# Kernel optimization log

Hardware: AMD Instinct MI355X
Metric: run time of the kernel (lower is better)

## Reference

```python
import jax, jax.numpy as jnp
import numpy as np

D_IN = 1024
D_OUT = 1024
N = 4096


def setup_inputs() -> dict:
    key = jax.random.key(0)
    kx, kq, kk, kv = jax.random.split(key, 4)
    x = jax.random.normal(kx, (N, D_IN), dtype=jnp.float32)
    # weights stored as [d_in, d_out] so that x @ W == torch Linear(x)
    s = 1.0 / np.sqrt(D_IN)
    W_q = jax.random.uniform(kq, (D_IN, D_OUT), jnp.float32, -s, s)
    W_k = jax.random.uniform(kk, (D_IN, D_OUT), jnp.float32, -s, s)
    W_v = jax.random.uniform(kv, (D_IN, D_OUT), jnp.float32, -s, s)
    return {"x": x, "W_q": W_q, "W_k": W_k, "W_v": W_v}


def reference(x, W_q, W_k, W_v):
    # x: [N, d_in]; projections -> [N, d_out]
    q = x @ W_q
    k = x @ W_k
    v = x @ W_v
    scale = 1.0 / jnp.sqrt(jnp.asarray(k.shape[-1], dtype=q.dtype))
    scores = (q @ k.T) * scale            # [N, N]
    weights = jax.nn.softmax(scores, axis=-1)
    return weights @ v                     # [N, d_out]
```

## Files before the change

kernel.cpp:

```cpp
#include <hip/hip_runtime.h>
#include <math.h>

typedef _Float16 f16;
typedef __attribute__((ext_vector_type(8))) _Float16 f16x8;
typedef __attribute__((ext_vector_type(4))) _Float16 f16x4;
typedef __attribute__((ext_vector_type(4))) float f32x4;

#define NSEQ 4096
#define DIN 1024
#define DOUT 1024

__device__ __forceinline__ void load16(const void* g, void* l) {
    __builtin_amdgcn_global_load_lds(
        (const __attribute__((address_space(1))) unsigned int*)g,
        (__attribute__((address_space(3))) unsigned int*)l, 16, 0, 0);
}

#define SB() __builtin_amdgcn_sched_barrier(0)
#define BARRIER() __builtin_amdgcn_s_barrier()

#define MM(I, J, KH, AR) \
    acc[I][J] = __builtin_amdgcn_mfma_f32_16x16x32_f16(AR[KH], b##J[KH], acc[I][J], 0, 0, 0)

#define MFMA16(I0, I1) \
    __builtin_amdgcn_s_setprio(1); \
    MM(I0,0,0,a0); MM(I0,1,0,a0); MM(I0,2,0,a0); MM(I0,3,0,a0); \
    MM(I1,0,0,a1); MM(I1,1,0,a1); MM(I1,2,0,a1); MM(I1,3,0,a1); \
    MM(I0,0,1,a0); MM(I0,1,1,a0); MM(I0,2,1,a0); MM(I0,3,1,a0); \
    MM(I1,0,1,a1); MM(I1,1,1,a1); MM(I1,2,1,a1); MM(I1,3,1,a1); \
    __builtin_amdgcn_s_setprio(0)

template <typename OutT, int EPI>
__global__ __launch_bounds__(512, 2)
void gemm8(const f16* __restrict__ A, const f16* __restrict__ B,
           OutT* __restrict__ c0, OutT* __restrict__ c1,
           OutT* __restrict__ c2, OutT* __restrict__ c3,
           int M, int N, int K, int lda, int ldb, int ldc, float scale,
           long aStrideZ, long bStrideZ, float* __restrict__ Sums)
{
    const int z = blockIdx.z;
    A += (long)z * aStrideZ;
    B += (long)z * bStrideZ;
    OutT* C = z == 0 ? c0 : (z == 1 ? c1 : (z == 2 ? c2 : c3));
    __shared__ f16 As[2 * 2 * 256 * 32];
    __shared__ f16 Bs[2 * 2 * 256 * 32];

    const int gx = gridDim.x;
    const int bid = blockIdx.y * gx + blockIdx.x;
    int bx, by;
    if (gx >= 8) {
        int xcd = bid & 7, s = bid >> 3;
        int px = s & 7, rest = s >> 3;
        int py = rest & 3, chunk = rest >> 2;
        int pg = xcd + (chunk << 3);
        int pcols = gx >> 3;
        int lp = 31 - __clz(pcols);
        bx = ((pg & (pcols - 1)) << 3) + px;
        by = ((pg >> lp) << 2) + py;
    } else {
        int nwg = gx * gridDim.y;
        int nb = (bid & 7) * (nwg >> 3) + (bid >> 3);
        bx = nb % gx; by = nb / gx;
    }

    const int t    = threadIdx.x;
    const int lane = t & 63;
    const int w    = t >> 6;
    const int wm   = (w >> 2) * 128;
    const int wn   = (w & 3) * 64;
    const int tile_m = by * 256;
    const int tile_n = bx * 256;
    const int quad = lane >> 4;
    const int l16  = lane & 15;
    const int srow = t >> 2;
    const int scol = (((t & 3) + srow + (srow >> 2)) & 3) * 8;
    const int qx16 = ((quad - (l16 + (l16 >> 2))) & 3) * 16;

    f32x4 acc[8][4];
#pragma unroll
    for (int i = 0; i < 8; i++)
#pragma unroll
        for (int j = 0; j < 4; j++) acc[i][j] = (f32x4){0.f, 0.f, 0.f, 0.f};

    const f16* Ag = A + (long)(tile_m + srow) * lda + scol;
    const f16* Bg = B + (long)(tile_n + srow) * ldb + scol;
    const long a128 = (long)128 * lda, b128 = (long)128 * ldb;
    char* AsW = (char*)As + t * 16;
    char* BsW = (char*)Bs + t * 16;
    const char* aRd = (const char*)As + (wm + l16) * 64 + qx16;
    const char* bRd = (const char*)Bs + (wn + l16) * 64 + qx16;

    auto stA = [&](int buf, int kh, int rb, int k0) {
        load16(Ag + k0 + kh * 32 + (long)rb * a128,
               AsW + buf * 32768 + kh * 16384 + rb * 8192);
    };
    auto stB = [&](int buf, int kh, int rb, int k0) {
        load16(Bg + k0 + kh * 32 + (long)rb * b128,
               BsW + buf * 32768 + kh * 16384 + rb * 8192);
    };

    const int nt = K >> 6;
    stA(0,0,0,0); stA(0,0,1,0); stA(0,1,0,0); stA(0,1,1,0);
    stB(0,0,0,0); stB(0,0,1,0); stB(0,1,0,0); stB(0,1,1,0);
    if (nt > 1) {
        stB(1,0,0,64); stB(1,0,1,64); stB(1,1,0,64); stB(1,1,1,64);
        asm volatile("s_waitcnt vmcnt(4)");
    } else {
        asm volatile("s_waitcnt vmcnt(0)");
    }
    SB(); BARRIER(); SB();

    for (int ti = 0; ti < nt; ++ti) {
        const int cur = ti & 1;
        const char* aR = aRd + cur * 32768;
        const char* bR = bRd + cur * 32768;
        const int k1 = (ti + 1) << 6;
        const int k2 = (ti + 2) << 6;
        f16x8 b0[2], b1[2], b2[2], b3[2], a0[2], a1[2];
        b0[0] = *(const f16x8*)(bR);          b1[0] = *(const f16x8*)(bR + 1024);
        b2[0] = *(const f16x8*)(bR + 2048);   b3[0] = *(const f16x8*)(bR + 3072);
        a0[0] = *(const f16x8*)(aR);          a1[0] = *(const f16x8*)(aR + 1024);
        b0[1] = *(const f16x8*)(bR + 16384);  b1[1] = *(const f16x8*)(bR + 17408);
        b2[1] = *(const f16x8*)(bR + 18432);  b3[1] = *(const f16x8*)(bR + 19456);
        a0[1] = *(const f16x8*)(aR + 16384);  a1[1] = *(const f16x8*)(aR + 17408);
        if (ti + 1 < nt) { stA(cur ^ 1, 0, 0, k1); stA(cur ^ 1, 0, 1, k1); }
        SB(); BARRIER();
        MFMA16(0, 1);
        BARRIER();
        a0[0] = *(const f16x8*)(aR + 2048);   a1[0] = *(const f16x8*)(aR + 3072);
        a0[1] = *(const f16x8*)(aR + 18432);  a1[1] = *(const f16x8*)(aR + 19456);
        if (ti + 1 < nt) { stA(cur ^ 1, 1, 0, k1); stA(cur ^ 1, 1, 1, k1); }
        SB(); BARRIER();
        MFMA16(2, 3);
        BARRIER();
        a0[0] = *(const f16x8*)(aR + 4096);   a1[0] = *(const f16x8*)(aR + 5120);
        a0[1] = *(const f16x8*)(aR + 20480);  a1[1] = *(const f16x8*)(aR + 21504);
        if (ti + 2 < nt) { stB(cur, 0, 0, k2); stB(cur, 0, 1, k2); }
        SB(); BARRIER();
        MFMA16(4, 5);
        BARRIER();
        a0[0] = *(const f16x8*)(aR + 6144);   a1[0] = *(const f16x8*)(aR + 7168);
        a0[1] = *(const f16x8*)(aR + 22528);  a1[1] = *(const f16x8*)(aR + 23552);
        if (ti + 2 < nt) { stB(cur, 1, 0, k2); stB(cur, 1, 1, k2); }
        SB(); BARRIER();
        MFMA16(6, 7);
        if (ti + 2 < nt)      asm volatile("s_waitcnt vmcnt(4)");
        else if (ti + 1 < nt) asm volatile("s_waitcnt vmcnt(0)");
        SB(); BARRIER(); SB();
    }

    if (EPI == 2) {
        const int bxs = bx * 4 + (wn >> 6);
#pragma unroll
        for (int i = 0; i < 8; i++) {
            float rs[4] = {0.f, 0.f, 0.f, 0.f};
#pragma unroll
            for (int j = 0; j < 4; j++)
#pragma unroll
                for (int r = 0; r < 4; r++) {
                    float e = __expf(acc[i][j][r] * scale);
                    int row = tile_m + wm + i * 16 + quad * 4 + r;
                    int col = tile_n + wn + j * 16 + l16;
                    C[(long)row * ldc + col] = (OutT)e;
                    rs[r] += e;
                }
#pragma unroll
            for (int msk = 1; msk < 16; msk <<= 1)
#pragma unroll
                for (int r = 0; r < 4; r++)
                    rs[r] += __shfl_xor(rs[r], msk, 64);
            if (l16 == 0)
#pragma unroll
                for (int r = 0; r < 4; r++) {
                    int row = tile_m + wm + i * 16 + quad * 4 + r;
                    Sums[(long)row * 64 + bxs] = rs[r];
                }
        }
    } else {
#pragma unroll
        for (int i = 0; i < 8; i++)
#pragma unroll
            for (int j = 0; j < 4; j++)
#pragma unroll
                for (int r = 0; r < 4; r++) {
                    int row = tile_m + wm + i * 16 + quad * 4 + r;
                    int col = tile_n + wn + j * 16 + l16;
                    C[(long)row * ldc + col] = (OutT)(acc[i][j][r] * scale);
                }
    }
}

template <typename OutT, int EPI>
__global__ __launch_bounds__(256, 2)
void gemm_bt(const f16* __restrict__ A, const f16* __restrict__ B,
             OutT* __restrict__ c0, OutT* __restrict__ c1,
             OutT* __restrict__ c2, OutT* __restrict__ c3,
             int M, int N, int K, int lda, int ldb, int ldc, float scale,
             long aStrideZ, long bStrideZ,
             f16* __restrict__ TC, int tz, int ldt, float* __restrict__ Sums)
{
    const int z = blockIdx.z;
    A += (long)z * aStrideZ;
    B += (long)z * bStrideZ;
    OutT* C = z == 0 ? c0 : (z == 1 ? c1 : (z == 2 ? c2 : c3));
    __shared__ f16 As[2 * 128 * 32];
    __shared__ f16 Bs[2 * 128 * 32];

    int gx = gridDim.x;
    int bid = blockIdx.y * gx + blockIdx.x;
    int xcd = bid & 7, s = bid >> 3;
    int px = s & 7, rest = s >> 3;
    int py = rest & 3, chunk = rest >> 2;
    int pg = xcd + (chunk << 3);
    int pcols = gx >> 3;
    int lp = 31 - __clz(pcols);
    int bx = ((pg & (pcols - 1)) << 3) + px;
    int by = ((pg >> lp) << 2) + py;

    const int t    = threadIdx.x;
    const int lane = t & 63;
    const int wave = t >> 6;
    const int wm   = (wave >> 1) * 64;
    const int wn   = (wave & 1) * 64;
    const int tile_m = by * 128;
    const int tile_n = bx * 128;
    const int quad = lane >> 4;
    const int l16  = lane & 15;
    const int srow = t >> 2;
    const int scol = (((t & 3) + srow + (srow >> 2)) & 3) * 8;
    const int qx8 = ((quad - (l16 + (l16 >> 2))) & 3) * 8;

    f32x4 acc[4][4];
#pragma unroll
    for (int i = 0; i < 4; i++)
#pragma unroll
        for (int j = 0; j < 4; j++)
            acc[i][j] = (f32x4){0.f, 0.f, 0.f, 0.f};

    const f16* Ab = A + (long)(tile_m + srow) * lda + scol;
    const f16* Bb = B + (long)(tile_n + srow) * ldb + scol;
    f16* Asd = As + t * 8;
    f16* Bsd = Bs + t * 8;

    for (int k0 = 0; k0 < K; k0 += 64) {
        load16(Ab + k0, Asd);
        load16(Ab + (long)64 * lda + k0, Asd + 2048);
        load16(Ab + k0 + 32, Asd + 4096);
        load16(Ab + (long)64 * lda + k0 + 32, Asd + 4096 + 2048);
        load16(Bb + k0, Bsd);
        load16(Bb + (long)64 * ldb + k0, Bsd + 2048);
        load16(Bb + k0 + 32, Bsd + 4096);
        load16(Bb + (long)64 * ldb + k0 + 32, Bsd + 4096 + 2048);
        __syncthreads();
#pragma unroll
        for (int p = 0; p < 2; p++) {
            f16x8 a[4], b[4];
#pragma unroll
            for (int i = 0; i < 4; i++)
                a[i] = *(const f16x8*)(As + p * 4096 + (wm + i * 16 + l16) * 32 + qx8);
#pragma unroll
            for (int j = 0; j < 4; j++)
                b[j] = *(const f16x8*)(Bs + p * 4096 + (wn + j * 16 + l16) * 32 + qx8);
#pragma unroll
            for (int i = 0; i < 4; i++)
#pragma unroll
                for (int j = 0; j < 4; j++)
                    acc[i][j] = __builtin_amdgcn_mfma_f32_16x16x32_f16(
                        a[i], b[j], acc[i][j], 0, 0, 0);
        }
        __syncthreads();
    }
    if (EPI == 1) {
        if (z == tz) {
#pragma unroll
            for (int i = 0; i < 4; i++)
#pragma unroll
                for (int j = 0; j < 4; j++) {
                    f16x4 o;
#pragma unroll
                    for (int r = 0; r < 4; r++) o[r] = (f16)(acc[i][j][r] * scale);
                    int row0 = tile_m + wm + i * 16 + quad * 4;
                    int col  = tile_n + wn + j * 16 + l16;
                    *(f16x4*)(TC + (long)col * ldt + row0) = o;
                }
        } else {
#pragma unroll
            for (int i = 0; i < 4; i++)
#pragma unroll
                for (int j = 0; j < 4; j++)
#pragma unroll
                    for (int r = 0; r < 4; r++) {
                        int row = tile_m + wm + i * 16 + quad * 4 + r;
                        int col = tile_n + wn + j * 16 + l16;
                        C[(long)row * ldc + col] = (OutT)(acc[i][j][r] * scale);
                    }
        }
    } else {
#pragma unroll
        for (int i = 0; i < 4; i++)
#pragma unroll
            for (int j = 0; j < 4; j++)
#pragma unroll
                for (int r = 0; r < 4; r++) {
                    int row = tile_m + wm + i * 16 + quad * 4 + r;
                    int col = tile_n + wn + j * 16 + l16;
                    C[(long)row * ldc + col] = (OutT)(acc[i][j][r] * scale);
                }
    }
}

__global__ void prep(const float* __restrict__ x,
                     const float* __restrict__ W0, const float* __restrict__ W1,
                     const float* __restrict__ W2,
                     f16* __restrict__ xb, f16* __restrict__ Wt) {
    if (blockIdx.z == 3) {
        long base = ((long)(blockIdx.y * 16 + blockIdx.x) * 256 + threadIdx.x) * 4;
#pragma unroll
        for (int it = 0; it < 16; it++) {
            long i = base + (long)it * (256 * 256 * 4);
            f32x4 v = *(const f32x4*)(x + i);
            f16x4 o;
            o.x = (f16)v.x; o.y = (f16)v.y; o.z = (f16)v.z; o.w = (f16)v.w;
            *(f16x4*)(xb + i) = o;
        }
        return;
    }
    __shared__ f16 tile[64][65];
    const float* W = blockIdx.z == 0 ? W0 : (blockIdx.z == 1 ? W1 : W2);
    f16* O = Wt + (long)blockIdx.z * DIN * DOUT;
    int r0 = blockIdx.y * 64;
    int c0 = blockIdx.x * 64;
    int tx = threadIdx.x & 63, ty = threadIdx.x >> 6;
#pragma unroll
    for (int i = 0; i < 16; i++)
        tile[ty + i * 4][tx] = (f16)W[(long)(r0 + ty + i * 4) * DOUT + c0 + tx];
    __syncthreads();
#pragma unroll
    for (int i = 0; i < 16; i++)
        O[(long)(c0 + ty + i * 4) * DIN + r0 + tx] = tile[tx][ty + i * 4];
}

__global__ __launch_bounds__(256)
void reduce_norm(const f16* __restrict__ p0, const f16* __restrict__ p1,
                 const f16* __restrict__ p2, const f16* __restrict__ p3,
                 const float* __restrict__ sums, float* __restrict__ out) {
    const int row = blockIdx.x;
    const int lane = threadIdx.x & 63;
    float s = sums[(long)row * 64 + lane];
#pragma unroll
    for (int msk = 1; msk < 64; msk <<= 1) s += __shfl_xor(s, msk, 64);
    const float inv = 1.f / s;
    long i = (long)row * 1024 + threadIdx.x * 4;
    f16x4 a = *(const f16x4*)(p0 + i);
    f16x4 b = *(const f16x4*)(p1 + i);
    f16x4 c = *(const f16x4*)(p2 + i);
    f16x4 d = *(const f16x4*)(p3 + i);
    f32x4 o;
    o.x = (((float)a.x + (float)b.x) + ((float)c.x + (float)d.x)) * inv;
    o.y = (((float)a.y + (float)b.y) + ((float)c.y + (float)d.y)) * inv;
    o.z = (((float)a.z + (float)b.z) + ((float)c.z + (float)d.z)) * inv;
    o.w = (((float)a.w + (float)b.w) + ((float)c.w + (float)d.w)) * inv;
    *(f32x4*)(out + i) = o;
}

extern "C" void kernel_launch(void* const* d_in, const int* in_sizes, int n_in,
                              void* d_out, int out_size, void* d_ws, size_t ws_size,
                              hipStream_t stream) {
    const float* x  = (const float*)d_in[0];
    const float* Wq = (const float*)d_in[1];
    const float* Wk = (const float*)d_in[2];
    const float* Wv = (const float*)d_in[3];
    float* out = (float*)d_out;
    char* ws = (char*)d_ws;
    const size_t MB = 1ull << 20;
    f16* xb  = (f16*)(ws);
    f16* Wt  = (f16*)(ws + 8 * MB);
    f16* Qb  = (f16*)(ws + 14 * MB);
    f16* Kb  = (f16*)(ws + 22 * MB);
    f16* Vt  = (f16*)(ws + 30 * MB);
    f16* S   = (f16*)(ws + 38 * MB);
    f16* scr0 = (f16*)(ws + 70 * MB);
    f16* scr1 = (f16*)(ws + 78 * MB);
    f16* scr2 = (f16*)(ws + 86 * MB);
    f16* scr3 = (f16*)(ws + 94 * MB);
    float* Sums = (float*)(ws);

    prep<<<dim3(16, 16, 4), 256, 0, stream>>>(x, Wq, Wk, Wv, xb, Wt);
    gemm_bt<f16, 1><<<dim3(8, 32, 3), 256, 0, stream>>>(
        xb, Wt, Qb, Kb, Qb, Qb, NSEQ, DOUT, DIN, DIN, DIN, DOUT, 1.0f,
        0, (long)DIN * DOUT, Vt, 2, NSEQ, nullptr);
    gemm8<f16, 2><<<dim3(16, 16, 1), 512, 0, stream>>>(
        Qb, Kb, S, S, S, S, NSEQ, NSEQ, DIN, DIN, DIN, NSEQ, 0.03125f,
        0, 0, Sums);
    gemm8<f16, 0><<<dim3(4, 16, 4), 512, 0, stream>>>(
        S, Vt, scr0, scr1, scr2, scr3, NSEQ, DOUT, 1024, NSEQ, NSEQ, DOUT, 1.0f,
        1024, 1024, nullptr);
    reduce_norm<<<4096, 256, 0, stream>>>(scr0, scr1, scr2, scr3, Sums, out);
}
```

Before: 198.3 us.

## Simplify GEMM pipeline to plain double buffering with one barrier per k-tile

Replaces the staggered prefetch schedule (A for the next tile and B two tiles ahead, interleaved between MFMA groups and separated by several barriers) with plain double buffering. All A and B loads for the next tile are issued at the top of each iteration, followed by a single wait and barrier at the end. Two extra A register sets alternate between MFMA groups so LDS reads can overlap the preceding MFMAs without intra-iteration barriers. The aim is to cut barrier and synchronisation overhead, at the cost of a shallower prefetch distance and more register pressure.

```diff
diff --git a/kernel.cpp b/kernel.cpp
--- a/kernel.cpp
+++ b/kernel.cpp
@@ -22,12 +22,12 @@
 #define MM(I, J, KH, AR) \
     acc[I][J] = __builtin_amdgcn_mfma_f32_16x16x32_f16(AR[KH], b##J[KH], acc[I][J], 0, 0, 0)
 
-#define MFMA16(I0, I1) \
+#define MFMA16(I0, I1, X, Y) \
     __builtin_amdgcn_s_setprio(1); \
-    MM(I0,0,0,a0); MM(I0,1,0,a0); MM(I0,2,0,a0); MM(I0,3,0,a0); \
-    MM(I1,0,0,a1); MM(I1,1,0,a1); MM(I1,2,0,a1); MM(I1,3,0,a1); \
-    MM(I0,0,1,a0); MM(I0,1,1,a0); MM(I0,2,1,a0); MM(I0,3,1,a0); \
-    MM(I1,0,1,a1); MM(I1,1,1,a1); MM(I1,2,1,a1); MM(I1,3,1,a1); \
+    MM(I0,0,0,X); MM(I0,1,0,X); MM(I0,2,0,X); MM(I0,3,0,X); \
+    MM(I1,0,0,Y); MM(I1,1,0,Y); MM(I1,2,0,Y); MM(I1,3,0,Y); \
+    MM(I0,0,1,X); MM(I0,1,1,X); MM(I0,2,1,X); MM(I0,3,1,X); \
+    MM(I1,0,1,Y); MM(I1,1,1,Y); MM(I1,2,1,Y); MM(I1,3,1,Y); \
     __builtin_amdgcn_s_setprio(0)
 
 template <typename OutT, int EPI>
@@ -102,12 +102,7 @@
     const int nt = K >> 6;
     stA(0,0,0,0); stA(0,0,1,0); stA(0,1,0,0); stA(0,1,1,0);
     stB(0,0,0,0); stB(0,0,1,0); stB(0,1,0,0); stB(0,1,1,0);
-    if (nt > 1) {
-        stB(1,0,0,64); stB(1,0,1,64); stB(1,1,0,64); stB(1,1,1,64);
-        asm volatile("s_waitcnt vmcnt(4)");
-    } else {
-        asm volatile("s_waitcnt vmcnt(0)");
-    }
+    asm volatile("s_waitcnt vmcnt(0)");
     SB(); BARRIER(); SB();
 
     for (int ti = 0; ti < nt; ++ti) {
@@ -115,37 +110,33 @@
         const char* aR = aRd + cur * 32768;
         const char* bR = bRd + cur * 32768;
         const int k1 = (ti + 1) << 6;
-        const int k2 = (ti + 2) << 6;
-        f16x8 b0[2], b1[2], b2[2], b3[2], a0[2], a1[2];
+        if (ti + 1 < nt) {
+            stA(cur ^ 1, 0, 0, k1); stA(cur ^ 1, 0, 1, k1);
+            stA(cur ^ 1, 1, 0, k1); stA(cur ^ 1, 1, 1, k1);
+            stB(cur ^ 1, 0, 0, k1); stB(cur ^ 1, 0, 1, k1);
+            stB(cur ^ 1, 1, 0, k1); stB(cur ^ 1, 1, 1, k1);
+        }
+        f16x8 b0[2], b1[2], b2[2], b3[2], a0[2], a1[2], a2[2], a3[2];
         b0[0] = *(const f16x8*)(bR);          b1[0] = *(const f16x8*)(bR + 1024);
         b2[0] = *(const f16x8*)(bR + 2048);   b3[0] = *(const f16x8*)(bR + 3072);
         a0[0] = *(const f16x8*)(aR);          a1[0] = *(const f16x8*)(aR + 1024);
         b0[1] = *(const f16x8*)(bR + 16384);  b1[1] = *(const f16x8*)(bR + 17408);
         b2[1] = *(const f16x8*)(bR + 18432);  b3[1] = *(const f16x8*)(bR + 19456);
         a0[1] = *(const f16x8*)(aR + 16384);  a1[1] = *(const f16x8*)(aR + 17408);
-        if (ti + 1 < nt) { stA(cur ^ 1, 0, 0, k1); stA(cur ^ 1, 0, 1, k1); }
-        SB(); BARRIER();
-        MFMA16(0, 1);
-        BARRIER();
-        a0[0] = *(const f16x8*)(aR + 2048);   a1[0] = *(const f16x8*)(aR + 3072);
-        a0[1] = *(const f16x8*)(aR + 18432);  a1[1] = *(const f16x8*)(aR + 19456);
-        if (ti + 1 < nt) { stA(cur ^ 1, 1, 0, k1); stA(cur ^ 1, 1, 1, k1); }
-        SB(); BARRIER();
-        MFMA16(2, 3);
-        BARRIER();
+        MFMA16(0, 1, a0, a1);
+        SB();
+        a2[0] = *(const f16x8*)(aR + 2048);   a3[0] = *(const f16x8*)(aR + 3072);
+        a2[1] = *(const f16x8*)(aR + 18432);  a3[1] = *(const f16x8*)(aR + 19456);
+        MFMA16(2, 3, a2, a3);
+        SB();
         a0[0] = *(const f16x8*)(aR + 4096);   a1[0] = *(const f16x8*)(aR + 5120);
         a0[1] = *(const f16x8*)(aR + 20480);  a1[1] = *(const f16x8*)(aR + 21504);
-        if (ti + 2 < nt) { stB(cur, 0, 0, k2); stB(cur, 0, 1, k2); }
-        SB(); BARRIER();
-        MFMA16(4, 5);
-        BARRIER();
-        a0[0] = *(const f16x8*)(aR + 6144);   a1[0] = *(const f16x8*)(aR + 7168);
-        a0[1] = *(const f16x8*)(aR + 22528);  a1[1] = *(const f16x8*)(aR + 23552);
-        if (ti + 2 < nt) { stB(cur, 1, 0, k2); stB(cur, 1, 1, k2); }
-        SB(); BARRIER();
-        MFMA16(6, 7);
-        if (ti + 2 < nt)      asm volatile("s_waitcnt vmcnt(4)");
-        else if (ti + 1 < nt) asm volatile("s_waitcnt vmcnt(0)");
+        MFMA16(4, 5, a0, a1);
+        SB();
+        a2[0] = *(const f16x8*)(aR + 6144);   a3[0] = *(const f16x8*)(aR + 7168);
+        a2[1] = *(const f16x8*)(aR + 22528);  a3[1] = *(const f16x8*)(aR + 23552);
+        MFMA16(6, 7, a2, a3);
+        if (ti + 1 < nt) asm volatile("s_waitcnt vmcnt(0)");
         SB(); BARRIER(); SB();
     }
 
```

After: 207.2 us. 1.04x slower.
